# Kernel optimization log

Measured on AMD Instinct MI355X. Metric: run time of the kernel, lower is better.

## Reference

```python
import jax, jax.numpy as jnp
import numpy as np

DEPTH = 3  # weights are SHARED across depth (same module object repeated in ModuleList)


def prelu(x, a):
    # nn.PReLU() with a single shared slope parameter
    return jnp.where(x >= 0, x, a * x)


def conv1x1(x, w, b):
    # x: (N,C,H,W), w: (O,C), b: (O,)
    return jnp.einsum('nchw,oc->nohw', x, w) + b[None, :, None, None]


def conv3x3(x, w, b):
    # w: (O,I,3,3), padding=1 stride=1 -> SAME
    y = jax.lax.conv_general_dilated(x, w, (1, 1), 'SAME',
                                     dimension_numbers=('NCHW', 'OIHW', 'NCHW'))
    return y + b[None, :, None, None]


def _unit(x, w1, b1, a1, w2, b2, a2, w3, b3, a3, wc, bc):
    # NonLocalAttention
    e1 = prelu(conv1x1(x, w1, b1), a1)   # (N,C,H,W)
    e2 = prelu(conv1x1(x, w2, b2), a2)   # (N,C,H,W)
    asm = prelu(conv1x1(x, w3, b3), a3)  # (N,C,H,W)
    N, C, H, W = e1.shape
    q = e1.reshape(N, C, H * W).transpose(0, 2, 1)     # (N,HW,C)
    k = e2.reshape(N, C, H * W)                        # (N,C,HW)
    score = jax.nn.softmax(jnp.matmul(q, k), axis=2)   # (N,HW,HW)
    v = asm.reshape(N, C, H * W).transpose(0, 2, 1)    # (N,HW,C)
    att = jnp.matmul(score, v).transpose(0, 2, 1).reshape(N, C, H, W)
    # Conv2d(channel, channel, 3, 1, 1) + exact GELU
    return jax.nn.gelu(conv3x3(att, wc, bc), approximate=False)


def setup_inputs() -> dict:
    key = jax.random.key(0)
    ks = jax.random.split(key, 8)
    C = 128
    x = jax.random.normal(ks[0], (1, C, 96, 96), dtype=jnp.float32)
    s = 0.05
    inp = {
        'x': x,
        'w1': jax.random.normal(ks[1], (C, C), jnp.float32) * s,
        'b1': jnp.zeros((C,), jnp.float32),
        'a1': jnp.float32(0.25),
        'w2': jax.random.normal(ks[2], (C, C), jnp.float32) * s,
        'b2': jnp.zeros((C,), jnp.float32),
        'a2': jnp.float32(0.25),
        'w3': jax.random.normal(ks[3], (C, C), jnp.float32) * s,
        'b3': jnp.zeros((C,), jnp.float32),
        'a3': jnp.float32(0.25),
        'wc': jax.random.normal(ks[4], (C, C, 3, 3), jnp.float32) * s,
        'bc': jnp.zeros((C,), jnp.float32),
    }
    return inp


def reference(x, w1, b1, a1, w2, b2, a2, w3, b3, a3, wc, bc):
    res = x
    for _ in range(DEPTH):  # same (shared) weights each iteration, per original module
        res = _unit(res, w1, b1, a1, w2, b2, a2, w3, b3, a3, wc, bc)
    return x + res
```

## Files before the change

### kernel.cpp

```cpp
#include <hip/hip_runtime.h>

#define HWPX 9216
#define NCH  128

typedef float  f32x4  __attribute__((ext_vector_type(4)));
typedef __bf16 bf16x8 __attribute__((ext_vector_type(8)));

#define SWZ16(row) ((((row) & 7) ^ (((row) >> 3) << 1)) << 4)

#define DPP_RED(v, OP)                                                         \
  do {                                                                         \
    v = OP(v, __int_as_float(__builtin_amdgcn_update_dpp(                      \
               0, __float_as_int(v), 0xB1, 0xF, 0xF, true)));                  \
    v = OP(v, __int_as_float(__builtin_amdgcn_update_dpp(                      \
               0, __float_as_int(v), 0x4E, 0xF, 0xF, true)));                  \
    v = OP(v, __int_as_float(__builtin_amdgcn_update_dpp(                      \
               0, __float_as_int(v), 0x124, 0xF, 0xF, true)));                 \
    v = OP(v, __int_as_float(__builtin_amdgcn_update_dpp(                      \
               0, __float_as_int(v), 0x128, 0xF, 0xF, true)));                 \
  } while (0)
__device__ __forceinline__ float op_max(float a, float b) { return fmaxf(a, b); }
__device__ __forceinline__ float op_add(float a, float b) { return a + b; }

__global__ __launch_bounds__(256) void prep_kernel(
    const float* __restrict__ w1, const float* __restrict__ w2,
    const float* __restrict__ w3, const float* __restrict__ wc,
    const float* __restrict__ x,
    __bf16* __restrict__ Wb, __bf16* __restrict__ wck,
    __bf16* __restrict__ Xb) {
  int tid = blockIdx.x * 256 + threadIdx.x;
  int nt  = gridDim.x * 256;
  for (int idx = tid; idx < 3 * 16384; idx += nt) {
    int j = idx >> 14;
    const float* w = (j == 0) ? w1 : (j == 1 ? w2 : w3);
    Wb[idx] = (__bf16)w[idx & 16383];
  }
  for (int idx = tid; idx < 147456; idx += nt) {
    int k = idx % 9;
    int rest = idx / 9;
    int c = rest & 127, o = rest >> 7;
    wck[(k * 128 + o) * 128 + c] = (__bf16)wc[idx];
  }
  for (int idx = tid; idx < 128 * HWPX; idx += nt) {
    int c = idx / HWPX, p = idx - c * HWPX;
    Xb[p * 128 + c] = (__bf16)x[idx];
  }
}

__global__ __launch_bounds__(256) void conv1x1_qkv(
    const __bf16* __restrict__ Xb, const __bf16* __restrict__ Wb,
    const float* __restrict__ b1, const float* __restrict__ b2,
    const float* __restrict__ b3, const float* __restrict__ a1,
    const float* __restrict__ a2, const float* __restrict__ a3,
    __bf16* __restrict__ Q, __bf16* __restrict__ K, __bf16* __restrict__ Vt) {
  const int tid = threadIdx.x, lane = tid & 63, w = tid >> 6;
  const int l16 = lane & 15, hi = lane >> 4;
  const int p0 = blockIdx.x * 64;
  const int z  = blockIdx.y;

  bf16x8 af[4][4];
#pragma unroll
  for (int pxt = 0; pxt < 4; ++pxt)
#pragma unroll
    for (int kc = 0; kc < 4; ++kc)
      af[pxt][kc] = *(const bf16x8*)&Xb[(p0 + pxt * 16 + l16) * 128 + kc * 32 + hi * 8];

  const int obase = w * 96 + z * 16;
  const int j = obase >> 7;
  const int oo = (obase & 127) + l16;
  bf16x8 bfg[4];
#pragma unroll
  for (int kc = 0; kc < 4; ++kc)
    bfg[kc] = *(const bf16x8*)&Wb[(obase + l16) * 128 + kc * 32 + hi * 8];
  f32x4 acc[4];
#pragma unroll
  for (int pxt = 0; pxt < 4; ++pxt) acc[pxt] = (f32x4){0.f, 0.f, 0.f, 0.f};
#pragma unroll
  for (int kc = 0; kc < 4; ++kc)
#pragma unroll
    for (int pxt = 0; pxt < 4; ++pxt)
      acc[pxt] = __builtin_amdgcn_mfma_f32_16x16x32_bf16(af[pxt][kc], bfg[kc], acc[pxt], 0, 0, 0);

  const float* bp = (j == 0) ? b1 : (j == 1 ? b2 : b3);
  const float bias = bp[oo];
  const float* ap = (j == 0) ? a1 : (j == 1 ? a2 : a3);
  const float sl = ap[0];
#pragma unroll
  for (int pxt = 0; pxt < 4; ++pxt)
#pragma unroll
    for (int r = 0; r < 4; ++r) {
      float v = acc[pxt][r] + bias;
      v = (v >= 0.f) ? v : sl * v;
      int px = p0 + pxt * 16 + hi * 4 + r;
      if (j == 0)      Q[px * 128 + oo] = (__bf16)v;
      else if (j == 1) K[px * 128 + oo] = (__bf16)v;
      else             Vt[oo * HWPX + px] = (__bf16)v;
    }
}

__global__ __launch_bounds__(512) void flash_attn(
    const __bf16* __restrict__ Q, const __bf16* __restrict__ Kb,
    const __bf16* __restrict__ Vt, float* __restrict__ Opart,
    float* __restrict__ mOut, float* __restrict__ lOut, int nt) {
  __shared__ __align__(16) unsigned char smem[81920];
  const int tid  = threadIdx.x;
  const int lane = tid & 63;
  const int w    = tid >> 6;
  const int l16  = lane & 15;
  const int hi   = lane >> 4;
  const int ord  = blockIdx.y * 72 + blockIdx.x;
  const int nsp  = gridDim.y;
  const int split = ord % nsp;
  const int qb   = (ord / nsp) * 128;
  const int kt0  = split * nt;

  const __bf16* gsrc[4];
  unsigned loff[4];
  long gstep;
  if (w < 4) {
    gstep = 8192;
#pragma unroll
    for (int j = 0; j < 4; ++j) {
      int seg = w * 4 + j;
      int row = seg * 4 + (lane >> 4);
      int ch  = lane & 15;
      gsrc[j] = Kb + (size_t)(kt0 * 64 + row) * 128 + (ch ^ (row & 7)) * 8;
      loff[j] = seg * 1024;
    }
  } else {
    gstep = 64;
#pragma unroll
    for (int j = 0; j < 4; ++j) {
      int seg = (w - 4) * 4 + j;
      int d  = seg * 8 + (lane >> 3);
      int ch = lane & 7;
      gsrc[j] = Vt + (size_t)d * HWPX + kt0 * 64 + (ch ^ (d & 7)) * 8;
      loff[j] = 16384 + seg * 1024;
    }
  }

#define STAGE(BUF) do {                                                        \
  _Pragma("unroll")                                                            \
  for (int j = 0; j < 4; ++j) {                                                \
    __builtin_amdgcn_global_load_lds(                                          \
        (const __attribute__((address_space(1))) unsigned int*)gsrc[j],        \
        (__attribute__((address_space(3))) unsigned int*)(smem + (BUF) * 32768 \
                                                          + loff[j]),          \
        16, 0, 0);                                                             \
    gsrc[j] += gstep;                                                          \
  } } while (0)

  bf16x8 qf[4];
  const int qrow = qb + w * 16 + l16;
#pragma unroll
  for (int dc = 0; dc < 4; ++dc)
    qf[dc] = *(const bf16x8*)&Q[qrow * 128 + dc * 32 + hi * 8];

  f32x4 oacc[8];
#pragma unroll
  for (int dc = 0; dc < 8; ++dc) oacc[dc] = (f32x4){0.f, 0.f, 0.f, 0.f};
  float m[4], l[4];
#pragma unroll
  for (int r = 0; r < 4; ++r) { m[r] = -INFINITY; l[r] = 0.f; }

  const unsigned pbase = 65536 + w * 2048;

  STAGE(0);
  __syncthreads();

  int cur = 0;
  for (int it = 0; it < nt; ++it) {
    if (it + 1 < nt) STAGE(cur ^ 1);

    const unsigned kb0 = cur * 32768;
    f32x4 s[4];
    __builtin_amdgcn_s_setprio(1);
#pragma unroll
    for (int g = 0; g < 4; ++g) {
      s[g] = (f32x4){0.f, 0.f, 0.f, 0.f};
      int row = g * 16 + l16;
#pragma unroll
      for (int dc = 0; dc < 4; ++dc) {
        bf16x8 kf = *(const bf16x8*)&smem[kb0 + row * 256 +
                        ((dc * 64 + hi * 16) ^ ((row & 7) << 4))];
        s[g] = __builtin_amdgcn_mfma_f32_16x16x32_bf16(qf[dc], kf, s[g], 0, 0, 0);
      }
    }
    __builtin_amdgcn_s_setprio(0);

    float mx[4];
#pragma unroll
    for (int r = 0; r < 4; ++r) {
      mx[r] = fmaxf(fmaxf(s[0][r], s[1][r]), fmaxf(s[2][r], s[3][r]));
      DPP_RED(mx[r], op_max);
    }
    bool need = false;
#pragma unroll
    for (int r = 0; r < 4; ++r) need = need || (mx[r] > m[r] + 8.f);
    if (__any(need)) {
#pragma unroll
      for (int r = 0; r < 4; ++r) {
        float mn = fmaxf(m[r], mx[r]);
        float alpha = __expf(m[r] - mn);
        m[r] = mn;
        l[r] *= alpha;
#pragma unroll
        for (int dc = 0; dc < 8; ++dc) oacc[dc][r] *= alpha;
      }
    }
    float rs[4];
#pragma unroll
    for (int r = 0; r < 4; ++r) rs[r] = 0.f;
#pragma unroll
    for (int g = 0; g < 4; ++g)
#pragma unroll
      for (int r = 0; r < 4; ++r) {
        float p = __expf(s[g][r] - m[r]);
        s[g][r] = p;
        rs[r] += p;
      }
#pragma unroll
    for (int r = 0; r < 4; ++r) {
      DPP_RED(rs[r], op_add);
      l[r] += rs[r];
    }

#pragma unroll
    for (int g = 0; g < 4; ++g)
#pragma unroll
      for (int r = 0; r < 4; ++r) {
        int row = hi * 4 + r;
        *(__bf16*)&smem[pbase + row * 128 +
                        ((g * 32 + l16 * 2) ^ SWZ16(row))] = (__bf16)s[g][r];
      }
    bf16x8 pa[2];
#pragma unroll
    for (int kc = 0; kc < 2; ++kc)
      pa[kc] = *(const bf16x8*)&smem[pbase + l16 * 128 +
                   ((kc * 64 + hi * 16) ^ SWZ16(l16))];
    __builtin_amdgcn_s_setprio(1);
#pragma unroll
    for (int dc = 0; dc < 8; ++dc) {
#pragma unroll
      for (int kc = 0; kc < 2; ++kc) {
        int row = dc * 16 + l16;
        bf16x8 vf = *(const bf16x8*)&smem[kb0 + 16384 + row * 128 +
                        ((kc * 64 + hi * 16) ^ ((row & 7) << 4))];
        oacc[dc] = __builtin_amdgcn_mfma_f32_16x16x32_bf16(pa[kc], vf, oacc[dc], 0, 0, 0);
      }
    }
    __builtin_amdgcn_s_setprio(0);
    __syncthreads();
    cur ^= 1;
  }
#undef STAGE

  const int sbase = split * HWPX;
#pragma unroll
  for (int dc = 0; dc < 8; ++dc)
#pragma unroll
    for (int r = 0; r < 4; ++r) {
      int q = qb + w * 16 + hi * 4 + r;
      Opart[(size_t)(sbase + q) * 128 + dc * 16 + l16] = oacc[dc][r];
    }
  if (l16 == 0) {
#pragma unroll
    for (int r = 0; r < 4; ++r) {
      int q = qb + w * 16 + hi * 4 + r;
      mOut[sbase + q] = m[r];
      lOut[sbase + q] = l[r];
    }
  }
}

__global__ __launch_bounds__(256) void flash_combine(
    const float* __restrict__ Opart, const float* __restrict__ mArr,
    const float* __restrict__ lArr, float* __restrict__ att, int ksplit) {
  int idx = blockIdx.x * 256 + threadIdx.x;
  int q = idx >> 5, d4 = idx & 31;
  float M = -INFINITY;
  for (int i = 0; i < ksplit; ++i) M = fmaxf(M, mArr[i * HWPX + q]);
  float denom = 0.f;
  f32x4 acc = (f32x4){0.f, 0.f, 0.f, 0.f};
  for (int i = 0; i < ksplit; ++i) {
    float wi = __expf(mArr[i * HWPX + q] - M);
    denom += lArr[i * HWPX + q] * wi;
    f32x4 v = *(const f32x4*)&Opart[((size_t)i * HWPX + q) * 128 + d4 * 4];
#pragma unroll
    for (int e = 0; e < 4; ++e) acc[e] += wi * v[e];
  }
  float inv = 1.f / denom;
  f32x4 r;
#pragma unroll
  for (int e = 0; e < 4; ++e) r[e] = acc[e] * inv;
  *(f32x4*)&att[(size_t)q * 128 + d4 * 4] = r;
}

__global__ __launch_bounds__(256) void conv3x3_gelu(
    const float* __restrict__ att, const __bf16* __restrict__ wck,
    const float* __restrict__ bc, const float* __restrict__ resid,
    float* __restrict__ out, __bf16* __restrict__ xbo) {
  __shared__ __align__(16) unsigned char smem[26112];
  const int tid = threadIdx.x;
  const int y   = blockIdx.x / 3;
  const int x0  = (blockIdx.x % 3) * 32;
  const int lane = tid & 63, w = tid >> 6;
  const int l16 = lane & 15, hi = lane >> 4;

  for (int id = tid; id < 1632; id += 256) {
    int px = id >> 4, ch = id & 15;
    int hy = px / 34, hx = px - hy * 34;
    int gy = y + hy - 1, gx = x0 + hx - 1;
    bf16x8 v;
    if (gy >= 0 && gy < 96 && gx >= 0 && gx < 96) {
      const float* src = &att[(gy * 96 + gx) * 128 + ch * 8];
      f32x4 aa = *(const f32x4*)src;
      f32x4 bb = *(const f32x4*)(src + 4);
#pragma unroll
      for (int e = 0; e < 4; ++e) { v[e] = (__bf16)aa[e]; v[4 + e] = (__bf16)bb[e]; }
    } else {
#pragma unroll
      for (int e = 0; e < 8; ++e) v[e] = (__bf16)0.f;
    }
    *(bf16x8*)&smem[px * 256 + ((ch * 16) ^ ((px & 7) << 4))] = v;
  }
  __syncthreads();

  f32x4 acc[2][2];
#pragma unroll
  for (int ot = 0; ot < 2; ++ot) {
    int obase = w * 32 + ot * 16 + hi * 4;
#pragma unroll
    for (int pt = 0; pt < 2; ++pt)
#pragma unroll
      for (int r = 0; r < 4; ++r) acc[ot][pt][r] = bc[obase + r];
  }

  for (int tap = 0; tap < 9; ++tap) {
    int dy = tap / 3, dx = tap - dy * 3;
#pragma unroll
    for (int cc = 0; cc < 4; ++cc) {
      bf16x8 af[2];
#pragma unroll
      for (int ot = 0; ot < 2; ++ot)
        af[ot] = *(const bf16x8*)&wck[(tap * 128 + w * 32 + ot * 16 + l16) * 128 +
                                      cc * 32 + hi * 8];
#pragma unroll
      for (int pt = 0; pt < 2; ++pt) {
        int px = dy * 34 + pt * 16 + l16 + dx;
        bf16x8 bf = *(const bf16x8*)&smem[px * 256 +
                        ((cc * 64 + hi * 16) ^ ((px & 7) << 4))];
#pragma unroll
        for (int ot = 0; ot < 2; ++ot)
          acc[ot][pt] = __builtin_amdgcn_mfma_f32_16x16x32_bf16(af[ot], bf, acc[ot][pt], 0, 0, 0);
      }
    }
  }

  float ge[2][2][4];
#pragma unroll
  for (int ot = 0; ot < 2; ++ot)
#pragma unroll
    for (int pt = 0; pt < 2; ++pt)
#pragma unroll
      for (int r = 0; r < 4; ++r) {
        float v = acc[ot][pt][r];
        ge[ot][pt][r] = 0.5f * v * (1.f + erff(v * 0.70710678118654752f));
      }

  if (xbo) {
    __syncthreads();
#pragma unroll
    for (int ot = 0; ot < 2; ++ot)
#pragma unroll
      for (int pt = 0; pt < 2; ++pt)
#pragma unroll
        for (int r = 0; r < 4; ++r) {
          int o  = w * 32 + ot * 16 + hi * 4 + r;
          int pl = pt * 16 + l16;
          *(__bf16*)&smem[pl * 256 + ((o * 2) ^ ((pl & 7) << 4))] =
              (__bf16)ge[ot][pt][r];
        }
    __syncthreads();
    for (int id = tid; id < 512; id += 256) {
      int pl = id >> 4, ch = id & 15;
      bf16x8 v = *(const bf16x8*)&smem[pl * 256 + ((ch * 16) ^ ((pl & 7) << 4))];
      *(bf16x8*)&xbo[(size_t)(y * 96 + x0 + pl) * 128 + ch * 8] = v;
    }
  } else {
#pragma unroll
    for (int ot = 0; ot < 2; ++ot)
#pragma unroll
      for (int pt = 0; pt < 2; ++pt)
#pragma unroll
        for (int r = 0; r < 4; ++r) {
          int o  = w * 32 + ot * 16 + hi * 4 + r;
          int px = y * 96 + x0 + pt * 16 + l16;
          out[o * HWPX + px] = ge[ot][pt][r] + resid[o * HWPX + px];
        }
  }
}

extern "C" void kernel_launch(void* const* d_in, const int* in_sizes, int n_in,
                              void* d_out, int out_size, void* d_ws, size_t ws_size,
                              hipStream_t stream) {
  const float* x  = (const float*)d_in[0];
  const float* w1 = (const float*)d_in[1];
  const float* b1 = (const float*)d_in[2];
  const float* a1 = (const float*)d_in[3];
  const float* w2 = (const float*)d_in[4];
  const float* b2 = (const float*)d_in[5];
  const float* a2 = (const float*)d_in[6];
  const float* w3 = (const float*)d_in[7];
  const float* b3 = (const float*)d_in[8];
  const float* a3 = (const float*)d_in[9];
  const float* wc = (const float*)d_in[10];
  const float* bc = (const float*)d_in[11];
  float* out = (float*)d_out;

  char* ws = (char*)d_ws;
  float*  att = (float*)(ws + 0);
  __bf16* Qb  = (__bf16*)(ws + 4718592);
  __bf16* Kb  = (__bf16*)(ws + 7077888);
  __bf16* Vt  = (__bf16*)(ws + 9437184);
  __bf16* Xb  = (__bf16*)(ws + 11796480);
  __bf16* Wb  = (__bf16*)(ws + 14155776);
  __bf16* wck = (__bf16*)(ws + 14254080);
  const size_t base_end = 14548992;

  int ksplit = 1;
  if (ws_size >= base_end + 8ull * (4718592 + 2 * 36864)) ksplit = 8;
  else if (ws_size >= base_end + 4ull * (4718592 + 2 * 36864)) ksplit = 4;
  else if (ws_size >= base_end + 2ull * (4718592 + 2 * 36864)) ksplit = 2;
  float* Opart = (float*)(ws + base_end);
  float* mArr  = (float*)(ws + base_end + (size_t)ksplit * 4718592);
  float* lArr  = (float*)(ws + base_end + (size_t)ksplit * (4718592 + 36864));

  prep_kernel<<<576, 256, 0, stream>>>(w1, w2, w3, wc, x, Wb, wck, Xb);

  for (int u = 0; u < 3; ++u) {
    conv1x1_qkv<<<dim3(144, 6), 256, 0, stream>>>(Xb, Wb, b1, b2, b3, a1, a2, a3,
                                                  Qb, Kb, Vt);
    flash_attn<<<dim3(72, ksplit), 512, 0, stream>>>(
        Qb, Kb, Vt, Opart, mArr, lArr, 144 / ksplit);
    flash_combine<<<1152, 256, 0, stream>>>(Opart, mArr, lArr, att, ksplit);
    conv3x3_gelu<<<288, 256, 0, stream>>>(att, wck, bc,
                                          (u == 2) ? x : nullptr,
                                          (u == 2) ? out : nullptr,
                                          (u < 2) ? Xb : nullptr);
  }
}
```

Measured before the change: 476.0 us.

## Give each flash-attention wave 32 query rows and store attention output as bf16

The flash attention kernel now runs 4 waves of 256 threads, each covering 32 query rows in two MFMA groups. Every K and V fragment read from LDS is therefore reused for two query tiles, which halves LDS traffic per MFMA. K stays double-buffered while V is single-buffered and staged after the PV step, using explicit vmcnt waits and barriers. Separately, the combine kernel writes bf16 instead of fp32, so the conv3x3 kernel loads bf16 directly and its conversion step is removed. The costs are higher register pressure per wave, fewer waves per block, and the V load now sits on the critical path each iteration.

```diff
diff --git a/kernel.cpp b/kernel.cpp
--- a/kernel.cpp
+++ b/kernel.cpp
@@ -5,6 +5,7 @@
 
 typedef float  f32x4  __attribute__((ext_vector_type(4)));
 typedef __bf16 bf16x8 __attribute__((ext_vector_type(8)));
+typedef __bf16 bf16x4 __attribute__((ext_vector_type(4)));
 
 #define SWZ16(row) ((((row) & 7) ^ (((row) >> 3) << 1)) << 4)
 
@@ -98,11 +99,11 @@
     }
 }
 
-__global__ __launch_bounds__(512) void flash_attn(
+__global__ __launch_bounds__(256) void flash_attn(
     const __bf16* __restrict__ Q, const __bf16* __restrict__ Kb,
     const __bf16* __restrict__ Vt, float* __restrict__ Opart,
     float* __restrict__ mOut, float* __restrict__ lOut, int nt) {
-  __shared__ __align__(16) unsigned char smem[81920];
+  __shared__ __align__(16) unsigned char smem[65536];
   const int tid  = threadIdx.x;
   const int lane = tid & 63;
   const int w    = tid >> 6;
@@ -114,168 +115,231 @@
   const int qb   = (ord / nsp) * 128;
   const int kt0  = split * nt;
 
-  const __bf16* gsrc[4];
-  unsigned loff[4];
-  long gstep;
-  if (w < 4) {
-    gstep = 8192;
-#pragma unroll
-    for (int j = 0; j < 4; ++j) {
-      int seg = w * 4 + j;
-      int row = seg * 4 + (lane >> 4);
-      int ch  = lane & 15;
-      gsrc[j] = Kb + (size_t)(kt0 * 64 + row) * 128 + (ch ^ (row & 7)) * 8;
-      loff[j] = seg * 1024;
-    }
-  } else {
-    gstep = 64;
-#pragma unroll
-    for (int j = 0; j < 4; ++j) {
-      int seg = (w - 4) * 4 + j;
-      int d  = seg * 8 + (lane >> 3);
-      int ch = lane & 7;
-      gsrc[j] = Vt + (size_t)d * HWPX + kt0 * 64 + (ch ^ (d & 7)) * 8;
-      loff[j] = 16384 + seg * 1024;
-    }
-  }
-
-#define STAGE(BUF) do {                                                        \
+  int koff[4], voff_ch;
+#pragma unroll
+  for (int j = 0; j < 4; ++j) {
+    int krow = w * 16 + j * 4 + hi;
+    koff[j] = krow * 128 + (((lane & 15) ^ (krow & 7)) * 8);
+  }
+  voff_ch = (((lane & 7) ^ ((lane >> 3) & 7)) * 8);
+
+#define STAGE_K(BUF, KT) do {                                                  \
+  _Pragma("unroll")                                                            \
+  for (int j = 0; j < 4; ++j)                                                  \
+    __builtin_amdgcn_global_load_lds(                                          \
+        (const __attribute__((address_space(1))) unsigned int*)                \
+            (Kb + (size_t)(KT) * 8192 + koff[j]),                              \
+        (__attribute__((address_space(3))) unsigned int*)                      \
+            (smem + (BUF) * 16384 + (w * 4 + j) * 1024),                       \
+        16, 0, 0);                                                             \
+  } while (0)
+
+#define STAGE_V(KT) do {                                                       \
   _Pragma("unroll")                                                            \
   for (int j = 0; j < 4; ++j) {                                                \
+    int vd = w * 32 + j * 8 + (lane >> 3);                                     \
     __builtin_amdgcn_global_load_lds(                                          \
-        (const __attribute__((address_space(1))) unsigned int*)gsrc[j],        \
-        (__attribute__((address_space(3))) unsigned int*)(smem + (BUF) * 32768 \
-                                                          + loff[j]),          \
+        (const __attribute__((address_space(1))) unsigned int*)                \
+            (Vt + (size_t)vd * HWPX + (size_t)(KT) * 64 + voff_ch),            \
+        (__attribute__((address_space(3))) unsigned int*)                      \
+            (smem + 32768 + (w * 4 + j) * 1024),                               \
         16, 0, 0);                                                             \
-    gsrc[j] += gstep;                                                          \
   } } while (0)
 
-  bf16x8 qf[4];
-  const int qrow = qb + w * 16 + l16;
-#pragma unroll
-  for (int dc = 0; dc < 4; ++dc)
-    qf[dc] = *(const bf16x8*)&Q[qrow * 128 + dc * 32 + hi * 8];
-
-  f32x4 oacc[8];
-#pragma unroll
-  for (int dc = 0; dc < 8; ++dc) oacc[dc] = (f32x4){0.f, 0.f, 0.f, 0.f};
-  float m[4], l[4];
-#pragma unroll
-  for (int r = 0; r < 4; ++r) { m[r] = -INFINITY; l[r] = 0.f; }
-
-  const unsigned pbase = 65536 + w * 2048;
-
-  STAGE(0);
-  __syncthreads();
+  bf16x8 qf[2][4];
+#pragma unroll
+  for (int g2 = 0; g2 < 2; ++g2) {
+    const int qrow = qb + w * 32 + g2 * 16 + l16;
+#pragma unroll
+    for (int dc = 0; dc < 4; ++dc)
+      qf[g2][dc] = *(const bf16x8*)&Q[qrow * 128 + dc * 32 + hi * 8];
+  }
+
+  f32x4 oacc[2][8];
+#pragma unroll
+  for (int g2 = 0; g2 < 2; ++g2)
+#pragma unroll
+    for (int dc = 0; dc < 8; ++dc) oacc[g2][dc] = (f32x4){0.f, 0.f, 0.f, 0.f};
+  float m[2][4], l[2][4];
+#pragma unroll
+  for (int g2 = 0; g2 < 2; ++g2)
+#pragma unroll
+    for (int r = 0; r < 4; ++r) { m[g2][r] = -INFINITY; l[g2][r] = 0.f; }
+
+  const unsigned pbase = 49152 + w * 4096;
+  f32x4 s[2][4];
+  bf16x8 pa[2][2];
+
+#define COMPUTE_QK(CUR)                                                        \
+  do {                                                                         \
+    const unsigned kb0 = (CUR) * 16384;                                        \
+    __builtin_amdgcn_s_setprio(1);                                             \
+    _Pragma("unroll")                                                          \
+    for (int g = 0; g < 4; ++g) {                                              \
+      int row = g * 16 + l16;                                                  \
+      bf16x8 kf[4];                                                            \
+      _Pragma("unroll")                                                        \
+      for (int dc = 0; dc < 4; ++dc)                                           \
+        kf[dc] = *(const bf16x8*)&smem[kb0 + row * 256 +                       \
+                     ((dc * 64 + hi * 16) ^ ((row & 7) << 4))];                \
+      _Pragma("unroll")                                                        \
+      for (int dc = 0; dc < 4; ++dc) {                                         \
+        s[0][g] = __builtin_amdgcn_mfma_f32_16x16x32_bf16(qf[0][dc], kf[dc],   \
+                                                          s[0][g], 0, 0, 0);   \
+        s[1][g] = __builtin_amdgcn_mfma_f32_16x16x32_bf16(qf[1][dc], kf[dc],   \
+                                                          s[1][g], 0, 0, 0);   \
+      }                                                                        \
+    }                                                                          \
+    __builtin_amdgcn_s_setprio(0);                                             \
+  } while (0)
+
+#define SOFTMAX_P()                                                            \
+  do {                                                                         \
+    float mx[2][4];                                                            \
+    bool need = false;                                                         \
+    _Pragma("unroll")                                                          \
+    for (int g2 = 0; g2 < 2; ++g2)                                             \
+      _Pragma("unroll")                                                        \
+      for (int r = 0; r < 4; ++r) {                                            \
+        float v = fmaxf(fmaxf(s[g2][0][r], s[g2][1][r]),                       \
+                        fmaxf(s[g2][2][r], s[g2][3][r]));                      \
+        DPP_RED(v, op_max);                                                    \
+        mx[g2][r] = v;                                                         \
+        need = need || (v > m[g2][r] + 8.f);                                   \
+      }                                                                        \
+    if (__any(need)) {                                                         \
+      _Pragma("unroll")                                                        \
+      for (int g2 = 0; g2 < 2; ++g2)                                           \
+        _Pragma("unroll")                                                      \
+        for (int r = 0; r < 4; ++r) {                                          \
+          float mn = fmaxf(m[g2][r], mx[g2][r]);                               \
+          float alpha = __expf(m[g2][r] - mn);                                 \
+          m[g2][r] = mn;                                                       \
+          l[g2][r] *= alpha;                                                   \
+          _Pragma("unroll")                                                    \
+          for (int dc = 0; dc < 8; ++dc) oacc[g2][dc][r] *= alpha;             \
+        }                                                                      \
+    }                                                                          \
+    _Pragma("unroll")                                                          \
+    for (int g2 = 0; g2 < 2; ++g2) {                                           \
+      float rs[4];                                                             \
+      _Pragma("unroll")                                                        \
+      for (int r = 0; r < 4; ++r) rs[r] = 0.f;                                 \
+      _Pragma("unroll")                                                        \
+      for (int g = 0; g < 4; ++g)                                              \
+        _Pragma("unroll")                                                      \
+        for (int r = 0; r < 4; ++r) {                                          \
+          float p = __expf(s[g2][g][r] - m[g2][r]);                            \
+          s[g2][g][r] = p;                                                     \
+          rs[r] += p;                                                          \
+        }                                                                      \
+      _Pragma("unroll")                                                        \
+      for (int r = 0; r < 4; ++r) {                                            \
+        DPP_RED(rs[r], op_add);                                                \
+        l[g2][r] += rs[r];                                                     \
+      }                                                                        \
+      _Pragma("unroll")                                                        \
+      for (int g = 0; g < 4; ++g)                                              \
+        _Pragma("unroll")                                                      \
+        for (int r = 0; r < 4; ++r) {                                          \
+          int row = g2 * 16 + hi * 4 + r;                                      \
+          *(__bf16*)&smem[pbase + row * 128 +                                  \
+                          ((g * 32 + l16 * 2) ^ SWZ16(row))] =                 \
+              (__bf16)s[g2][g][r];                                             \
+        }                                                                      \
+    }                                                                          \
+    _Pragma("unroll")                                                          \
+    for (int g2 = 0; g2 < 2; ++g2) {                                           \
+      int row = g2 * 16 + l16;                                                 \
+      _Pragma("unroll")                                                        \
+      for (int kc = 0; kc < 2; ++kc)                                           \
+        pa[g2][kc] = *(const bf16x8*)&smem[pbase + row * 128 +                 \
+                         ((kc * 64 + hi * 16) ^ SWZ16(row))];                  \
+    }                                                                          \
+  } while (0)
+
+#define COMPUTE_PV()                                                           \
+  do {                                                                         \
+    __builtin_amdgcn_s_setprio(1);                                             \
+    _Pragma("unroll")                                                          \
+    for (int dc = 0; dc < 8; ++dc) {                                           \
+      int row = dc * 16 + l16;                                                 \
+      _Pragma("unroll")                                                        \
+      for (int kc = 0; kc < 2; ++kc) {                                         \
+        bf16x8 vf = *(const bf16x8*)&smem[32768 + row * 128 +                  \
+                        ((kc * 64 + hi * 16) ^ ((row & 7) << 4))];             \
+        oacc[0][dc] = __builtin_amdgcn_mfma_f32_16x16x32_bf16(                 \
+            pa[0][kc], vf, oacc[0][dc], 0, 0, 0);                              \
+        oacc[1][dc] = __builtin_amdgcn_mfma_f32_16x16x32_bf16(                 \
+            pa[1][kc], vf, oacc[1][dc], 0, 0, 0);                              \
+      }                                                                        \
+    }                                                                          \
+    __builtin_amdgcn_s_setprio(0);                                             \
+  } while (0)
+
+  STAGE_K(0, kt0);
+  STAGE_V(kt0);
+  asm volatile("s_waitcnt vmcnt(0)" ::: "memory");
+  __builtin_amdgcn_s_barrier();
 
   int cur = 0;
-  for (int it = 0; it < nt; ++it) {
-    if (it + 1 < nt) STAGE(cur ^ 1);
-
-    const unsigned kb0 = cur * 32768;
-    f32x4 s[4];
-    __builtin_amdgcn_s_setprio(1);
-#pragma unroll
-    for (int g = 0; g < 4; ++g) {
-      s[g] = (f32x4){0.f, 0.f, 0.f, 0.f};
-      int row = g * 16 + l16;
-#pragma unroll
-      for (int dc = 0; dc < 4; ++dc) {
-        bf16x8 kf = *(const bf16x8*)&smem[kb0 + row * 256 +
-                        ((dc * 64 + hi * 16) ^ ((row & 7) << 4))];
-        s[g] = __builtin_amdgcn_mfma_f32_16x16x32_bf16(qf[dc], kf, s[g], 0, 0, 0);
+  for (int it = 0; it < nt - 1; ++it) {
+    STAGE_K(cur ^ 1, kt0 + it + 1);
+#pragma unroll
+    for (int g2 = 0; g2 < 2; ++g2)
+#pragma unroll
+      for (int g = 0; g < 4; ++g) s[g2][g] = (f32x4){0.f, 0.f, 0.f, 0.f};
+    COMPUTE_QK(cur);
+    SOFTMAX_P();
+    asm volatile("s_waitcnt vmcnt(4)" ::: "memory");
+    __builtin_amdgcn_s_barrier();
+    COMPUTE_PV();
+    asm volatile("s_waitcnt vmcnt(0)" ::: "memory");
+    __builtin_amdgcn_s_barrier();
+    STAGE_V(kt0 + it + 1);
+    cur ^= 1;
+  }
+#pragma unroll
+  for (int g2 = 0; g2 < 2; ++g2)
+#pragma unroll
+    for (int g = 0; g < 4; ++g) s[g2][g] = (f32x4){0.f, 0.f, 0.f, 0.f};
+  COMPUTE_QK(cur);
+  SOFTMAX_P();
+  asm volatile("s_waitcnt vmcnt(0)" ::: "memory");
+  __builtin_amdgcn_s_barrier();
+  COMPUTE_PV();
+
+#undef STAGE_K
+#undef STAGE_V
+#undef COMPUTE_QK
+#undef SOFTMAX_P
+#undef COMPUTE_PV
+
+  const int sbase = split * HWPX;
+#pragma unroll
+  for (int g2 = 0; g2 < 2; ++g2)
+#pragma unroll
+    for (int dc = 0; dc < 8; ++dc)
+#pragma unroll
+      for (int r = 0; r < 4; ++r) {
+        int q = qb + w * 32 + g2 * 16 + hi * 4 + r;
+        Opart[(size_t)(sbase + q) * 128 + dc * 16 + l16] = oacc[g2][dc][r];
       }
-    }
-    __builtin_amdgcn_s_setprio(0);
-
-    float mx[4];
-#pragma unroll
-    for (int r = 0; r < 4; ++r) {
-      mx[r] = fmaxf(fmaxf(s[0][r], s[1][r]), fmaxf(s[2][r], s[3][r]));
-      DPP_RED(mx[r], op_max);
-    }
-    bool need = false;
-#pragma unroll
-    for (int r = 0; r < 4; ++r) need = need || (mx[r] > m[r] + 8.f);
-    if (__any(need)) {
+  if (l16 == 0) {
+#pragma unroll
+    for (int g2 = 0; g2 < 2; ++g2)
 #pragma unroll
       for (int r = 0; r < 4; ++r) {
-        float mn = fmaxf(m[r], mx[r]);
-        float alpha = __expf(m[r] - mn);
-        m[r] = mn;
-        l[r] *= alpha;
-#pragma unroll
-        for (int dc = 0; dc < 8; ++dc) oacc[dc][r] *= alpha;
+        int q = qb + w * 32 + g2 * 16 + hi * 4 + r;
+        mOut[sbase + q] = m[g2][r];
+        lOut[sbase + q] = l[g2][r];
       }
-    }
-    float rs[4];
-#pragma unroll
-    for (int r = 0; r < 4; ++r) rs[r] = 0.f;
-#pragma unroll
-    for (int g = 0; g < 4; ++g)
-#pragma unroll
-      for (int r = 0; r < 4; ++r) {
-        float p = __expf(s[g][r] - m[r]);
-        s[g][r] = p;
-        rs[r] += p;
-      }
-#pragma unroll
-    for (int r = 0; r < 4; ++r) {
-      DPP_RED(rs[r], op_add);
-      l[r] += rs[r];
-    }
-
-#pragma unroll
-    for (int g = 0; g < 4; ++g)
-#pragma unroll
-      for (int r = 0; r < 4; ++r) {
-        int row = hi * 4 + r;
-        *(__bf16*)&smem[pbase + row * 128 +
-                        ((g * 32 + l16 * 2) ^ SWZ16(row))] = (__bf16)s[g][r];
-      }
-    bf16x8 pa[2];
-#pragma unroll
-    for (int kc = 0; kc < 2; ++kc)
-      pa[kc] = *(const bf16x8*)&smem[pbase + l16 * 128 +
-                   ((kc * 64 + hi * 16) ^ SWZ16(l16))];
-    __builtin_amdgcn_s_setprio(1);
-#pragma unroll
-    for (int dc = 0; dc < 8; ++dc) {
-#pragma unroll
-      for (int kc = 0; kc < 2; ++kc) {
-        int row = dc * 16 + l16;
-        bf16x8 vf = *(const bf16x8*)&smem[kb0 + 16384 + row * 128 +
-                        ((kc * 64 + hi * 16) ^ ((row & 7) << 4))];
-        oacc[dc] = __builtin_amdgcn_mfma_f32_16x16x32_bf16(pa[kc], vf, oacc[dc], 0, 0, 0);
-      }
-    }
-    __builtin_amdgcn_s_setprio(0);
-    __syncthreads();
-    cur ^= 1;
-  }
-#undef STAGE
-
-  const int sbase = split * HWPX;
-#pragma unroll
-  for (int dc = 0; dc < 8; ++dc)
-#pragma unroll
-    for (int r = 0; r < 4; ++r) {
-      int q = qb + w * 16 + hi * 4 + r;
-      Opart[(size_t)(sbase + q) * 128 + dc * 16 + l16] = oacc[dc][r];
-    }
-  if (l16 == 0) {
-#pragma unroll
-    for (int r = 0; r < 4; ++r) {
-      int q = qb + w * 16 + hi * 4 + r;
-      mOut[sbase + q] = m[r];
-      lOut[sbase + q] = l[r];
-    }
   }
 }
 
 __global__ __launch_bounds__(256) void flash_combine(
     const float* __restrict__ Opart, const float* __restrict__ mArr,
-    const float* __restrict__ lArr, float* __restrict__ att, int ksplit) {
+    const float* __restrict__ lArr, __bf16* __restrict__ attb, int ksplit) {
   int idx = blockIdx.x * 256 + threadIdx.x;
   int q = idx >> 5, d4 = idx & 31;
   float M = -INFINITY;
@@ -290,14 +354,14 @@
     for (int e = 0; e < 4; ++e) acc[e] += wi * v[e];
   }
   float inv = 1.f / denom;
-  f32x4 r;
-#pragma unroll
-  for (int e = 0; e < 4; ++e) r[e] = acc[e] * inv;
-  *(f32x4*)&att[(size_t)q * 128 + d4 * 4] = r;
+  bf16x4 r;
+#pragma unroll
+  for (int e = 0; e < 4; ++e) r[e] = (__bf16)(acc[e] * inv);
+  *(bf16x4*)&attb[(size_t)q * 128 + d4 * 4] = r;
 }
 
 __global__ __launch_bounds__(256) void conv3x3_gelu(
-    const float* __restrict__ att, const __bf16* __restrict__ wck,
+    const __bf16* __restrict__ attb, const __bf16* __restrict__ wck,
     const float* __restrict__ bc, const float* __restrict__ resid,
     float* __restrict__ out, __bf16* __restrict__ xbo) {
   __shared__ __align__(16) unsigned char smem[26112];
@@ -313,11 +377,7 @@
     int gy = y + hy - 1, gx = x0 + hx - 1;
     bf16x8 v;
     if (gy >= 0 && gy < 96 && gx >= 0 && gx < 96) {
-      const float* src = &att[(gy * 96 + gx) * 128 + ch * 8];
-      f32x4 aa = *(const f32x4*)src;
-      f32x4 bb = *(const f32x4*)(src + 4);
-#pragma unroll
-      for (int e = 0; e < 4; ++e) { v[e] = (__bf16)aa[e]; v[4 + e] = (__bf16)bb[e]; }
+      v = *(const bf16x8*)&attb[(size_t)(gy * 96 + gx) * 128 + ch * 8];
     } else {
 #pragma unroll
       for (int e = 0; e < 8; ++e) v[e] = (__bf16)0.f;
@@ -419,14 +479,14 @@
   float* out = (float*)d_out;
 
   char* ws = (char*)d_ws;
-  float*  att = (float*)(ws + 0);
-  __bf16* Qb  = (__bf16*)(ws + 4718592);
-  __bf16* Kb  = (__bf16*)(ws + 7077888);
-  __bf16* Vt  = (__bf16*)(ws + 9437184);
-  __bf16* Xb  = (__bf16*)(ws + 11796480);
-  __bf16* Wb  = (__bf16*)(ws + 14155776);
-  __bf16* wck = (__bf16*)(ws + 14254080);
-  const size_t base_end = 14548992;
+  __bf16* attb = (__bf16*)(ws + 0);
+  __bf16* Qb  = (__bf16*)(ws + 2359296);
+  __bf16* Kb  = (__bf16*)(ws + 4718592);
+  __bf16* Vt  = (__bf16*)(ws + 7077888);
+  __bf16* Xb  = (__bf16*)(ws + 9437184);
+  __bf16* Wb  = (__bf16*)(ws + 11796480);
+  __bf16* wck = (__bf16*)(ws + 11894784);
+  const size_t base_end = 12189696;
 
   int ksplit = 1;
   if (ws_size >= base_end + 8ull * (4718592 + 2 * 36864)) ksplit = 8;
@@ -441,10 +501,10 @@
   for (int u = 0; u < 3; ++u) {
     conv1x1_qkv<<<dim3(144, 6), 256, 0, stream>>>(Xb, Wb, b1, b2, b3, a1, a2, a3,
                                                   Qb, Kb, Vt);
-    flash_attn<<<dim3(72, ksplit), 512, 0, stream>>>(
+    flash_attn<<<dim3(72, ksplit), 256, 0, stream>>>(
         Qb, Kb, Vt, Opart, mArr, lArr, 144 / ksplit);
-    flash_combine<<<1152, 256, 0, stream>>>(Opart, mArr, lArr, att, ksplit);
-    conv3x3_gelu<<<288, 256, 0, stream>>>(att, wck, bc,
+    flash_combine<<<1152, 256, 0, stream>>>(Opart, mArr, lArr, attb, ksplit);
+    conv3x3_gelu<<<288, 256, 0, stream>>>(attb, wck, bc,
                                           (u == 2) ? x : nullptr,
                                           (u == 2) ? out : nullptr,
                                           (u < 2) ? Xb : nullptr);
```

Measured after the change: 593.8 us. 24.8% more time.
